# Optimization experiments

Measured on AMD Instinct MI355X. Metric: run time of the kernel, lower is better.

Reference implementation:

```python
import jax, jax.numpy as jnp
import numpy as np
from jax import lax

D = 64; B = 8; P = 16; E = P * (P - 1); C = 5; N = 256
H = 4; HD = D // H; NB = 5; NL = 2; NCLASSES = 8; NTYPES = 7


def _gelu(x):
    return jax.nn.gelu(x, approximate=False)


def _ln(x, g, b, eps=1e-5):
    m = x.mean(-1, keepdims=True)
    v = ((x - m) ** 2).mean(-1, keepdims=True)
    return (x - m) * lax.rsqrt(v + eps) * g + b


def _gn(x, g, b, groups=8, eps=1e-5):
    # x: [M, d, L]; GroupNorm over (channels_in_group, L)
    M, d, L = x.shape
    xg = x.reshape(M, groups, -1)
    m = xg.mean(-1, keepdims=True)
    v = ((xg - m) ** 2).mean(-1, keepdims=True)
    xg = (xg - m) * lax.rsqrt(v + eps)
    return xg.reshape(M, d, L) * g[None, :, None] + b[None, :, None]


def _forward(edge_data, edge_types, edge_mask, p, x_idx, y_idx, params):
    (stem_w, stem_b, conv_w, gn_g, gn_b, type_emb, em_w, em_b, em_g, em_bt,
     a_wqkv, a_bqkv, a_wo, a_bo, ln1_g, ln1_b, ff_w1, ff_b1, ff_w2, ff_b2,
     ln2_g, ln2_b, eh_w, eh_b, nm_w, nm_b, nm_g, nm_bt, nh_w, nh_b) = params
    Bq, Eq, Cq, Nq = edge_data.shape
    # --- EdgeFeatureExtractor: stem linear + 5 residual conv blocks + avg pool ---
    x = edge_data.reshape(Bq * Eq, Cq, Nq)
    h = jnp.einsum('mcn,cd->mdn', x, stem_w) + stem_b[None, :, None]  # [BE, d, N]
    for i in range(conv_w.shape[0]):
        c = lax.conv_general_dilated(h, conv_w[i], (1,), ((1, 1),),
                                     dimension_numbers=('NCH', 'OIH', 'NCH'))
        h = h + _gelu(_gn(c, gn_g[i], gn_b[i]))
    emb = h.mean(-1).reshape(Bq, Eq, D)  # adaptive avg pool to 1
    # --- type embedding + 2-input merge ---
    temb = type_emb[edge_types]
    emb = _gelu(_ln(jnp.concatenate([emb, temb], -1) @ em_w + em_b, em_g, em_bt))
    # --- 2 self-attention layers (post-LN) ---
    pad = ~edge_mask
    neg = jnp.asarray(-1e9, emb.dtype)
    scale = np.float32(1.0 / np.sqrt(HD))
    for l in range(a_wqkv.shape[0]):
        qkv = emb @ a_wqkv[l] + a_bqkv[l]
        q, k, v = jnp.split(qkv, 3, axis=-1)
        q = q.reshape(Bq, Eq, H, HD).transpose(0, 2, 1, 3)
        k = k.reshape(Bq, Eq, H, HD).transpose(0, 2, 1, 3)
        v = v.reshape(Bq, Eq, H, HD).transpose(0, 2, 1, 3)
        s = jnp.einsum('bhqd,bhkd->bhqk', q, k) * scale
        s = jnp.where(pad[:, None, None, :], neg, s)
        a = jax.nn.softmax(s, axis=-1)
        o = jnp.einsum('bhqk,bhkd->bhqd', a, v).transpose(0, 2, 1, 3).reshape(Bq, Eq, D)
        o = o @ a_wo[l] + a_bo[l]
        emb = _ln(emb + o, ln1_g[l], ln1_b[l])
        f = _gelu(emb @ ff_w1[l] + ff_b1[l]) @ ff_w2[l] + ff_b2[l]
        emb = _ln(emb + f, ln2_g[l], ln2_b[l])
    edge_logits = emb @ eh_w + eh_b  # [B, E, 2]
    # --- node heads: vectorized version of the per-node dict gather ---
    # edge_order[u, v] = u*(p-1) + v - (v > u)
    others = np.array([i for i in range(p) if i not in (x_idx, y_idx)], dtype=np.int64)

    def eidx(u, v):
        u = np.asarray(u); v = np.asarray(v)
        return u * (p - 1) + v - (v > u).astype(np.int64)

    i_ux = eidx(others, x_idx)
    i_uy = eidx(others, y_idx)
    i_xu = eidx(x_idx, others)
    i_yu = eidx(y_idx, others)
    g = jnp.concatenate([emb[:, i_ux], emb[:, i_uy], emb[:, i_xu], emb[:, i_yu]], axis=-1)  # [B, p-2, 4d]
    node = _gelu(_ln(g @ nm_w + nm_b, nm_g, nm_bt))
    node_logits = node @ nh_w + nh_b  # [B, p-2, 8]
    return edge_logits, node_logits


def setup_inputs() -> dict:
    key = jax.random.key(0)
    ks = iter(jax.random.split(key, 64))

    def rn(shape, s=0.05):
        return jax.random.normal(next(ks), shape, jnp.float32) * s

    return {
        'edge_data': jax.random.normal(next(ks), (B, E, C, N), jnp.float32),
        'edge_types': jax.random.randint(next(ks), (B, E), 0, NTYPES),
        'edge_mask': jnp.ones((B, E), dtype=bool),
        'p': P, 'x_idx': 0, 'y_idx': 1,
        'stem_w': rn((C, D)), 'stem_b': jnp.zeros((D,)),
        'conv_w': rn((NB, D, D, 3)), 'gn_g': jnp.ones((NB, D)), 'gn_b': jnp.zeros((NB, D)),
        'type_emb': rn((NTYPES, D), 1.0),
        'em_w': rn((2 * D, D)), 'em_b': jnp.zeros((D,)), 'em_g': jnp.ones((D,)), 'em_bt': jnp.zeros((D,)),
        'a_wqkv': rn((NL, D, 3 * D)), 'a_bqkv': jnp.zeros((NL, 3 * D)),
        'a_wo': rn((NL, D, D)), 'a_bo': jnp.zeros((NL, D)),
        'ln1_g': jnp.ones((NL, D)), 'ln1_b': jnp.zeros((NL, D)),
        'ff_w1': rn((NL, D, 4 * D)), 'ff_b1': jnp.zeros((NL, 4 * D)),
        'ff_w2': rn((NL, 4 * D, D)), 'ff_b2': jnp.zeros((NL, D)),
        'ln2_g': jnp.ones((NL, D)), 'ln2_b': jnp.zeros((NL, D)),
        'eh_w': rn((D, 2)), 'eh_b': jnp.zeros((2,)),
        'nm_w': rn((4 * D, D)), 'nm_b': jnp.zeros((D,)), 'nm_g': jnp.ones((D,)), 'nm_bt': jnp.zeros((D,)),
        'nh_w': rn((D, NCLASSES)), 'nh_b': jnp.zeros((NCLASSES,)),
    }


def reference(edge_data, edge_types, edge_mask, p, x_idx, y_idx, stem_w, stem_b,
              conv_w, gn_g, gn_b, type_emb, em_w, em_b, em_g, em_bt,
              a_wqkv, a_bqkv, a_wo, a_bo, ln1_g, ln1_b, ff_w1, ff_b1, ff_w2, ff_b2,
              ln2_g, ln2_b, eh_w, eh_b, nm_w, nm_b, nm_g, nm_bt, nh_w, nh_b):
    params = (stem_w, stem_b, conv_w, gn_g, gn_b, type_emb, em_w, em_b, em_g, em_bt,
              a_wqkv, a_bqkv, a_wo, a_bo, ln1_g, ln1_b, ff_w1, ff_b1, ff_w2, ff_b2,
              ln2_g, ln2_b, eh_w, eh_b, nm_w, nm_b, nm_g, nm_bt, nh_w, nh_b)
    return _forward(edge_data, edge_types, edge_mask, int(p), int(x_idx), int(y_idx), params)
```

## Files before the change

kernel.cpp:

```cpp
#include <hip/hip_runtime.h>
#include <hip/hip_bf16.h>
#include <math.h>

#define NEDGE 240
#define NBAT  8
#define MROWS 1920
#define NPTS  256
#define CIN   5

typedef __attribute__((ext_vector_type(8))) short  bf16x8;
typedef __attribute__((ext_vector_type(4))) float  f32x4;

__device__ __forceinline__ float gelu_f(float x){
    float x2 = x*x;
    float t  = fmaf(0.07135481f, x2, 1.59576912f);
    float s  = fminf(x*t, 80.f);
    float e  = __expf(s);
    float r  = __builtin_amdgcn_rcpf(e + 1.0f);
    return x*e*r;
}
__device__ __forceinline__ float wave_sum(float v){
    #pragma unroll
    for (int off=32; off>0; off>>=1) v += __shfl_xor(v, off);
    return v;
}
__device__ __forceinline__ unsigned short f2bf(float x){
    unsigned int u = __float_as_uint(x);
    return (unsigned short)((u + 0x7FFFu + ((u>>16)&1u)) >> 16);
}
__device__ __forceinline__ unsigned pack_bf2(float lo, float hi){
    __hip_bfloat162 t = __float22bfloat162_rn(make_float2(lo, hi));
    union { __hip_bfloat162 b; unsigned u; } cv; cv.b = t;
    return cv.u;
}

__global__ __launch_bounds__(256) void k_wprep(
    const float* __restrict__ conv_w, unsigned short* __restrict__ wf)
{
    int t = blockIdx.x*256 + threadIdx.x;
    if (t >= 120*64) return;
    int lane = t & 63, f = t >> 6;
    int q = f & 1, tap = (f>>1)%3, ob = (f/6)&3, layer = f/24;
    int o = 16*ob + (lane&15);
    int ibase = 32*q + 8*(lane>>4);
    #pragma unroll
    for (int e=0;e<8;++e){
        int i = ibase + e;
        float w = conv_w[(((size_t)layer*64 + o)*64 + i)*3 + tap];
        wf[(size_t)t*8 + e] = f2bf(w);
    }
}

__global__ __launch_bounds__(512, 2) void k_extract(
    const float* __restrict__ edge_data, const float* __restrict__ stem_w,
    const float* __restrict__ stem_b, const unsigned short* __restrict__ wf,
    const float* __restrict__ gn_g, const float* __restrict__ gn_b,
    float* __restrict__ emb0)
{
    __shared__ unsigned short hbf[258*64];
    __shared__ float redg[8][2][2];
    __shared__ float redp[8][16];
    __shared__ float gnp[640];
    const int m = blockIdx.x, tid = threadIdx.x;
    const int w = tid>>6, lane = tid&63;
    const int g = (lane>>4)&3, l15 = lane&15;
    const int wb = w&3, colbase = 128*(w>>2);
    const bf16x8* wfp = (const bf16x8*)wf;

    bf16x8 A[6];
    #pragma unroll
    for (int fq=0; fq<6; ++fq)
        A[fq] = wfp[(size_t)((wb*3)*2 + fq)*64 + lane];

    for (int i=tid; i<640; i+=512) gnp[i] = (i<320) ? gn_g[i] : gn_b[i-320];

    float h[8][4];

    {
        const float* xs = edge_data + (size_t)m*CIN*NPTS;
        float sw[4][6];
        #pragma unroll
        for (int j=0;j<4;++j){
            int o = 16*wb + 4*g + j;
            #pragma unroll
            for (int c=0;c<5;++c) sw[j][c] = stem_w[c*64+o];
            sw[j][5] = stem_b[o];
        }
        #pragma unroll
        for (int nbl=0;nbl<8;++nbl){
            int n = colbase + 16*nbl + l15;
            float x0=xs[n], x1=xs[NPTS+n], x2=xs[2*NPTS+n],
                  x3=xs[3*NPTS+n], x4=xs[4*NPTS+n];
            #pragma unroll
            for (int j=0;j<4;++j)
                h[nbl][j] = sw[j][5] + x0*sw[j][0] + x1*sw[j][1]
                          + x2*sw[j][2] + x3*sw[j][3] + x4*sw[j][4];
            int np = n + 1;
            #pragma unroll
            for (int jp=0;jp<2;++jp){
                int i0 = 16*wb + 4*g + 2*jp;
                unsigned off = (unsigned)(np*128 + (((i0>>3)^(np&7))<<4) + ((i0&7)<<1));
                *(unsigned*)((char*)hbf + off) = pack_bf2(h[nbl][2*jp], h[nbl][2*jp+1]);
            }
        }
    }
    if (tid < 32)       ((unsigned int*)hbf)[tid] = 0u;
    else if (tid < 64)  ((unsigned int*)hbf)[257*32 + tid - 32] = 0u;
    __syncthreads();

    #pragma unroll 1
    for (int layer=0; layer<5; ++layer){
        f32x4 acc[8];
        #pragma unroll
        for (int nbl=0;nbl<8;++nbl) acc[nbl] = (f32x4){0.f,0.f,0.f,0.f};

        #pragma unroll
        for (int tap=0; tap<3; ++tap)
        #pragma unroll
        for (int q=0; q<2; ++q){
            #pragma unroll
            for (int nbl=0;nbl<8;++nbl){
                int np = colbase + 16*nbl + l15 + tap;
                unsigned off = (unsigned)(np*128 + (((4*q+g)^(np&7))<<4));
                bf16x8 Bv = *(const bf16x8*)((const char*)hbf + off);
                acc[nbl] = __builtin_amdgcn_mfma_f32_16x16x32_bf16(
                               A[tap*2+q], Bv, acc[nbl], 0,0,0);
            }
        }

        float s=0.f, sq=0.f;
        #pragma unroll
        for (int nbl=0;nbl<8;++nbl)
            #pragma unroll
            for (int j=0;j<4;++j){ float v=acc[nbl][j]; s+=v; sq+=v*v; }
        #pragma unroll
        for (int off=1; off<=16; off<<=1){
            s  += __shfl_xor(s,  off);
            sq += __shfl_xor(sq, off);
        }
        if ((lane&31)==0){
            redg[w][lane>>5][0] = s;
            redg[w][lane>>5][1] = sq;
        }
        __syncthreads();

        if (layer < 4){
            #pragma unroll
            for (int fq=0; fq<6; ++fq)
                A[fq] = wfp[(size_t)((layer+1)*24 + (wb*3)*2 + fq)*64 + lane];
        }

        int hf = g>>1;
        float S = redg[wb][hf][0] + redg[wb+4][hf][0];
        float Q = redg[wb][hf][1] + redg[wb+4][hf][1];
        float mu = S*(1.f/2048.f);
        float rstd = rsqrtf(Q*(1.f/2048.f) - mu*mu + 1e-5f);

        float gg[4], bb[4];
        #pragma unroll
        for (int j=0;j<4;++j){
            int o = 16*wb + 4*g + j;
            gg[j] = gnp[layer*64+o]; bb[j] = gnp[320+layer*64+o];
        }
        #pragma unroll
        for (int nbl=0;nbl<8;++nbl)
            #pragma unroll
            for (int j=0;j<4;++j){
                float xn = (acc[nbl][j]-mu)*rstd*gg[j] + bb[j];
                h[nbl][j] += gelu_f(xn);
            }
        if (layer < 4){
            #pragma unroll
            for (int nbl=0;nbl<8;++nbl){
                int np = colbase + 16*nbl + l15 + 1;
                #pragma unroll
                for (int jp=0;jp<2;++jp){
                    int i0 = 16*wb + 4*g + 2*jp;
                    unsigned off = (unsigned)(np*128 + (((i0>>3)^(np&7))<<4) + ((i0&7)<<1));
                    *(unsigned*)((char*)hbf + off) = pack_bf2(h[nbl][2*jp], h[nbl][2*jp+1]);
                }
            }
            __syncthreads();
        }
    }

    float p[4];
    #pragma unroll
    for (int j=0;j<4;++j){
        float a = 0.f;
        #pragma unroll
        for (int nbl=0;nbl<8;++nbl) a += h[nbl][j];
        p[j] = a;
    }
    #pragma unroll
    for (int off=1; off<=8; off<<=1)
        #pragma unroll
        for (int j=0;j<4;++j) p[j] += __shfl_xor(p[j], off);
    if (l15==0){
        #pragma unroll
        for (int j=0;j<4;++j) redp[w][4*g+j] = p[j];
    }
    __syncthreads();
    if (tid < 64){
        int ob = tid>>4, r = tid&15;
        emb0[(size_t)m*64+tid] = (redp[ob][r] + redp[ob+4][r]) * (1.0f/256.0f);
    }
}

__global__ __launch_bounds__(256) void k_mergeqkv(
    const float* __restrict__ emb0, const int* __restrict__ edge_types,
    const float* __restrict__ type_emb, const float* __restrict__ em_w,
    const float* __restrict__ em_b, const float* __restrict__ em_g,
    const float* __restrict__ em_bt, const float* __restrict__ wqkv,
    const float* __restrict__ bqkv, float* __restrict__ emb,
    float* __restrict__ qkv)
{
    int m  = blockIdx.x*4 + (threadIdx.x>>6);
    int ln = threadIdx.x & 63;
    float a = emb0[(size_t)m*64+ln];
    int ty = edge_types[m];
    float tb = type_emb[ty*64+ln];
    float v = em_b[ln];
    for (int j=0;j<64;++j) v += __shfl(a,j)  * em_w[j*64+ln];
    for (int j=0;j<64;++j) v += __shfl(tb,j) * em_w[(64+j)*64+ln];
    float mu  = wave_sum(v)*(1.0f/64.0f);
    float d   = v - mu;
    float var = wave_sum(d*d)*(1.0f/64.0f);
    float e = gelu_f(d * rsqrtf(var+1e-5f) * em_g[ln] + em_bt[ln]);
    emb[(size_t)m*64+ln] = e;
    float q = bqkv[ln], k = bqkv[64+ln], vv = bqkv[128+ln];
    for (int j=0;j<64;++j){
        float ej = __shfl(e,j);
        q  += ej*wqkv[j*192+ln];
        k  += ej*wqkv[j*192+64+ln];
        vv += ej*wqkv[j*192+128+ln];
    }
    qkv[(size_t)m*192+ln]=q; qkv[(size_t)m*192+64+ln]=k; qkv[(size_t)m*192+128+ln]=vv;
}

__global__ __launch_bounds__(256) void k_attn(
    const float* __restrict__ qkv, float* __restrict__ o)
{
    __shared__ float Ks[NEDGE][16], Vs[NEDGE][16];
    int b = blockIdx.x >> 2, h = blockIdx.x & 3;
    int tid = threadIdx.x;
    for (int i=tid; i<NEDGE*16; i+=256){
        int r = i>>4, c = i&15;
        size_t base = ((size_t)(b*NEDGE+r))*192 + h*16 + c;
        Ks[r][c] = qkv[base+64];
        Vs[r][c] = qkv[base+128];
    }
    __syncthreads();
    if (tid < NEDGE){
        float qv[16];
        size_t qb = ((size_t)(b*NEDGE+tid))*192 + h*16;
        #pragma unroll
        for (int d=0; d<16; ++d) qv[d] = qkv[qb+d];
        float mx = -3e38f, l = 0.f, acc[16];
        #pragma unroll
        for (int d=0; d<16; ++d) acc[d]=0.f;
        for (int key=0; key<NEDGE; ++key){
            float s=0.f;
            #pragma unroll
            for (int d=0; d<16; ++d) s += qv[d]*Ks[key][d];
            s *= 0.25f;
            if (s > mx){
                float so = __expf(mx - s);
                l *= so;
                #pragma unroll
                for (int d=0; d<16; ++d) acc[d] *= so;
                mx = s;
            }
            float pp = __expf(s - mx);
            l += pp;
            #pragma unroll
            for (int d=0; d<16; ++d) acc[d] = fmaf(pp, Vs[key][d], acc[d]);
        }
        float inv = 1.f/l;
        size_t obase = ((size_t)(b*NEDGE+tid))*64 + h*16;
        #pragma unroll
        for (int d=0; d<16; ++d) o[obase+d] = acc[d]*inv;
    }
}

__global__ __launch_bounds__(256) void k_postattn(
    const float* __restrict__ o, const float* __restrict__ wo,
    const float* __restrict__ bo, const float* __restrict__ g1,
    const float* __restrict__ b1ln, const float* __restrict__ w1,
    const float* __restrict__ b1, const float* __restrict__ w2,
    const float* __restrict__ b2, const float* __restrict__ g2,
    const float* __restrict__ b2ln, float* __restrict__ emb,
    const float* __restrict__ wqkv, const float* __restrict__ bqkv,
    float* __restrict__ qkv)
{
    int m  = blockIdx.x*4 + (threadIdx.x>>6);
    int ln = threadIdx.x & 63;
    float ov = o[(size_t)m*64+ln];
    float r = bo[ln];
    for (int j=0;j<64;++j) r += __shfl(ov,j)*wo[j*64+ln];
    float x = emb[(size_t)m*64+ln] + r;
    float mu  = wave_sum(x)*(1.f/64.f);
    float d   = x-mu;
    float var = wave_sum(d*d)*(1.f/64.f);
    float e1 = d*rsqrtf(var+1e-5f)*g1[ln] + b1ln[ln];
    float h[4];
    #pragma unroll
    for (int u=0;u<4;++u) h[u]=b1[ln*4+u];
    for (int j=0;j<64;++j){
        float ej = __shfl(e1,j);
        const float* wr = w1 + j*256 + ln*4;
        #pragma unroll
        for (int u=0;u<4;++u) h[u] += ej*wr[u];
    }
    #pragma unroll
    for (int u=0;u<4;++u) h[u]=gelu_f(h[u]);
    float f = b2[ln];
    #pragma unroll
    for (int u=0;u<4;++u){
        for (int j=0;j<64;++j)
            f += __shfl(h[u],j) * w2[(j*4+u)*64+ln];
    }
    float x2 = e1 + f;
    float mu2  = wave_sum(x2)*(1.f/64.f);
    float d2   = x2-mu2;
    float var2 = wave_sum(d2*d2)*(1.f/64.f);
    float e2 = d2*rsqrtf(var2+1e-5f)*g2[ln] + b2ln[ln];
    emb[(size_t)m*64+ln] = e2;
    if (wqkv){
        float q = bqkv[ln], k = bqkv[64+ln], vv = bqkv[128+ln];
        for (int j=0;j<64;++j){
            float ej = __shfl(e2,j);
            q  += ej*wqkv[j*192+ln];
            k  += ej*wqkv[j*192+64+ln];
            vv += ej*wqkv[j*192+128+ln];
        }
        qkv[(size_t)m*192+ln]=q; qkv[(size_t)m*192+64+ln]=k; qkv[(size_t)m*192+128+ln]=vv;
    }
}

__global__ __launch_bounds__(256) void k_heads(
    const float* __restrict__ emb, const float* __restrict__ eh_w,
    const float* __restrict__ eh_b, const float* __restrict__ nm_w,
    const float* __restrict__ nm_b, const float* __restrict__ nm_g,
    const float* __restrict__ nm_bt, const float* __restrict__ nh_w,
    const float* __restrict__ nh_b, const int* __restrict__ pp,
    const int* __restrict__ xp, const int* __restrict__ yp,
    float* __restrict__ out)
{
    if (blockIdx.x < 15){
        int gid = blockIdx.x*256 + threadIdx.x;
        int m = gid>>1, c = gid&1;
        float s = eh_b[c];
        const float* e = emb + (size_t)m*64;
        #pragma unroll 8
        for (int j=0;j<64;++j) s += e[j]*eh_w[j*2+c];
        out[gid] = s;
        return;
    }
    int wid = (blockIdx.x-15)*4 + (threadIdx.x>>6);
    int ln  = threadIdx.x & 63;
    int p = pp[0], xi = xp[0], yi = yp[0];
    int nu = p-2;
    if (wid >= NBAT*nu) return;
    int b = wid / nu, r = wid % nu;
    int u=-1, cnt=0;
    for (int i=0;i<p;++i){ if (i!=xi && i!=yi){ if (cnt==r){u=i;break;} ++cnt; } }
    #define EIDX(a,v) ((a)*(p-1) + (v) - (((v)>(a))?1:0))
    int iux = EIDX(u,xi), iuy = EIDX(u,yi), ixu = EIDX(xi,u), iyu = EIDX(yi,u);
    float g0 = emb[((size_t)(b*NEDGE+iux))*64+ln];
    float g1 = emb[((size_t)(b*NEDGE+iuy))*64+ln];
    float g2 = emb[((size_t)(b*NEDGE+ixu))*64+ln];
    float g3 = emb[((size_t)(b*NEDGE+iyu))*64+ln];
    float v = nm_b[ln];
    for (int j=0;j<64;++j) v += __shfl(g0,j)*nm_w[j*64+ln];
    for (int j=0;j<64;++j) v += __shfl(g1,j)*nm_w[(64+j)*64+ln];
    for (int j=0;j<64;++j) v += __shfl(g2,j)*nm_w[(128+j)*64+ln];
    for (int j=0;j<64;++j) v += __shfl(g3,j)*nm_w[(192+j)*64+ln];
    float mu  = wave_sum(v)*(1.f/64.f);
    float d   = v-mu;
    float var = wave_sum(d*d)*(1.f/64.f);
    float node = gelu_f(d*rsqrtf(var+1e-5f)*nm_g[ln] + nm_bt[ln]);
    float pl[8];
    #pragma unroll
    for (int c=0;c<8;++c) pl[c] = node*nh_w[ln*8+c];
    #pragma unroll
    for (int off=32; off>0; off>>=1)
        #pragma unroll
        for (int c=0;c<8;++c) pl[c] += __shfl_xor(pl[c], off);
    if (ln==0){
        #pragma unroll
        for (int c=0;c<8;++c) out[MROWS*2 + ((size_t)wid)*8 + c] = pl[c] + nh_b[c];
    }
}

extern "C" void kernel_launch(void* const* d_in, const int* in_sizes, int n_in,
                              void* d_out, int out_size, void* d_ws, size_t ws_size,
                              hipStream_t stream)
{
    const float* edge_data = (const float*)d_in[0];
    const int*   edge_types= (const int*)d_in[1];
    const int* pp = (const int*)d_in[3];
    const int* xp = (const int*)d_in[4];
    const int* yp = (const int*)d_in[5];
    const float* stem_w=(const float*)d_in[6];
    const float* stem_b=(const float*)d_in[7];
    const float* conv_w=(const float*)d_in[8];
    const float* gn_g=(const float*)d_in[9];
    const float* gn_b=(const float*)d_in[10];
    const float* type_emb=(const float*)d_in[11];
    const float* em_w=(const float*)d_in[12];
    const float* em_b=(const float*)d_in[13];
    const float* em_g=(const float*)d_in[14];
    const float* em_bt=(const float*)d_in[15];
    const float* a_wqkv=(const float*)d_in[16];
    const float* a_bqkv=(const float*)d_in[17];
    const float* a_wo=(const float*)d_in[18];
    const float* a_bo=(const float*)d_in[19];
    const float* ln1_g=(const float*)d_in[20];
    const float* ln1_b=(const float*)d_in[21];
    const float* ff_w1=(const float*)d_in[22];
    const float* ff_b1=(const float*)d_in[23];
    const float* ff_w2=(const float*)d_in[24];
    const float* ff_b2=(const float*)d_in[25];
    const float* ln2_g=(const float*)d_in[26];
    const float* ln2_b=(const float*)d_in[27];
    const float* eh_w=(const float*)d_in[28];
    const float* eh_b=(const float*)d_in[29];
    const float* nm_w=(const float*)d_in[30];
    const float* nm_b=(const float*)d_in[31];
    const float* nm_g=(const float*)d_in[32];
    const float* nm_bt=(const float*)d_in[33];
    const float* nh_w=(const float*)d_in[34];
    const float* nh_b=(const float*)d_in[35];
    (void)in_sizes; (void)n_in; (void)out_size; (void)ws_size;

    unsigned short* wfrag = (unsigned short*)d_ws;
    float* wsf  = (float*)d_ws;
    float* emb  = wsf + 30720;
    float* qkvb = emb + 122880;
    float* obuf = qkvb + 368640;
    float* outp = (float*)d_out;

    k_wprep   <<<30, 256, 0, stream>>>(conv_w, wfrag);
    k_extract <<<MROWS, 512, 0, stream>>>(edge_data, stem_w, stem_b, wfrag, gn_g, gn_b, emb);
    k_mergeqkv<<<MROWS/4, 256, 0, stream>>>(emb, edge_types, type_emb, em_w, em_b, em_g,
                                            em_bt, a_wqkv, a_bqkv, emb, qkvb);
    k_attn    <<<NBAT*4, 256, 0, stream>>>(qkvb, obuf);
    k_postattn<<<MROWS/4, 256, 0, stream>>>(obuf, a_wo, a_bo, ln1_g, ln1_b,
                                            ff_w1, ff_b1, ff_w2, ff_b2, ln2_g, ln2_b,
                                            emb, a_wqkv + (size_t)64*192, a_bqkv + 192, qkvb);
    k_attn    <<<NBAT*4, 256, 0, stream>>>(qkvb, obuf);
    k_postattn<<<MROWS/4, 256, 0, stream>>>(obuf, a_wo + (size_t)64*64, a_bo + 64,
                                            ln1_g + 64, ln1_b + 64,
                                            ff_w1 + (size_t)64*256, ff_b1 + 256,
                                            ff_w2 + (size_t)256*64, ff_b2 + 64,
                                            ln2_g + 64, ln2_b + 64,
                                            emb, (const float*)nullptr, (const float*)nullptr, qkvb);
    k_heads   <<<43, 256, 0, stream>>>(emb, eh_w, eh_b, nm_w, nm_b, nm_g, nm_bt,
                                       nh_w, nh_b, pp, xp, yp, outp);
}
```

Before: 305.8 us.

## Split attention keys across lanes and streamline extract/post-attention kernels

The attention kernel now launches four times as many blocks. Each query is handled by four lanes that each scan a quarter of the keys, and their online-softmax states are merged with shuffles. K and V are stored transposed in shared memory. The conv extract kernel precomputes swizzled LDS addresses, writes 64-bit packed bf16 stores, moves the next layer's weight prefetch before the reduction barrier, and folds the GroupNorm affine into a single FMA. The merge and post-attention kernels split their dot-product accumulators and use float4 weight loads to shorten dependency chains; the transposed layout may add some LDS bank conflicts.

New measurement: 249.4 us. 18.4% less time.

```diff
diff --git a/kernel.cpp b/kernel.cpp
--- a/kernel.cpp
+++ b/kernel.cpp
@@ -70,9 +70,22 @@
     bf16x8 A[6];
     #pragma unroll
     for (int fq=0; fq<6; ++fq)
-        A[fq] = wfp[(size_t)((wb*3)*2 + fq)*64 + lane];
+        A[fq] = wfp[(size_t)(wb*6 + fq)*64 + lane];
 
     for (int i=tid; i<640; i+=512) gnp[i] = (i<320) ? gn_g[i] : gn_b[i-320];
+
+    const int i0 = 16*wb + 4*g;
+    unsigned raddr[3][2];
+    {
+        unsigned clb = (unsigned)((colbase + l15)*128);
+        #pragma unroll
+        for (int tap=0;tap<3;++tap)
+            #pragma unroll
+            for (int q=0;q<2;++q)
+                raddr[tap][q] = clb + (unsigned)(((4*q+g) ^ ((l15+tap)&7))<<4);
+    }
+    const unsigned wb0 = (unsigned)((colbase + l15 + 1)*128
+                       + (((i0>>3) ^ ((l15+1)&7))<<4) + ((i0&7)<<1));
 
     float h[8][4];
 
@@ -81,7 +94,7 @@
         float sw[4][6];
         #pragma unroll
         for (int j=0;j<4;++j){
-            int o = 16*wb + 4*g + j;
+            int o = i0 + j;
             #pragma unroll
             for (int c=0;c<5;++c) sw[j][c] = stem_w[c*64+o];
             sw[j][5] = stem_b[o];
@@ -95,13 +108,9 @@
             for (int j=0;j<4;++j)
                 h[nbl][j] = sw[j][5] + x0*sw[j][0] + x1*sw[j][1]
                           + x2*sw[j][2] + x3*sw[j][3] + x4*sw[j][4];
-            int np = n + 1;
-            #pragma unroll
-            for (int jp=0;jp<2;++jp){
-                int i0 = 16*wb + 4*g + 2*jp;
-                unsigned off = (unsigned)(np*128 + (((i0>>3)^(np&7))<<4) + ((i0&7)<<1));
-                *(unsigned*)((char*)hbf + off) = pack_bf2(h[nbl][2*jp], h[nbl][2*jp+1]);
-            }
+            unsigned long long pk = (unsigned long long)pack_bf2(h[nbl][0], h[nbl][1])
+                                  | ((unsigned long long)pack_bf2(h[nbl][2], h[nbl][3]) << 32);
+            *(unsigned long long*)((char*)hbf + wb0 + 2048*nbl) = pk;
         }
     }
     if (tid < 32)       ((unsigned int*)hbf)[tid] = 0u;
@@ -120,14 +129,19 @@
         for (int q=0; q<2; ++q){
             #pragma unroll
             for (int nbl=0;nbl<8;++nbl){
-                int np = colbase + 16*nbl + l15 + tap;
-                unsigned off = (unsigned)(np*128 + (((4*q+g)^(np&7))<<4));
-                bf16x8 Bv = *(const bf16x8*)((const char*)hbf + off);
+                bf16x8 Bv = *(const bf16x8*)((const char*)hbf
+                              + raddr[tap][q] + (2048*nbl + 128*tap));
                 acc[nbl] = __builtin_amdgcn_mfma_f32_16x16x32_bf16(
                                A[tap*2+q], Bv, acc[nbl], 0,0,0);
             }
         }
 
+        if (layer < 4){
+            #pragma unroll
+            for (int fq=0; fq<6; ++fq)
+                A[fq] = wfp[(size_t)((layer+1)*24 + wb*6 + fq)*64 + lane];
+        }
+
         float s=0.f, sq=0.f;
         #pragma unroll
         for (int nbl=0;nbl<8;++nbl)
@@ -143,12 +157,6 @@
             redg[w][lane>>5][1] = sq;
         }
         __syncthreads();
-
-        if (layer < 4){
-            #pragma unroll
-            for (int fq=0; fq<6; ++fq)
-                A[fq] = wfp[(size_t)((layer+1)*24 + (wb*3)*2 + fq)*64 + lane];
-        }
 
         int hf = g>>1;
         float S = redg[wb][hf][0] + redg[wb+4][hf][0];
@@ -156,29 +164,26 @@
         float mu = S*(1.f/2048.f);
         float rstd = rsqrtf(Q*(1.f/2048.f) - mu*mu + 1e-5f);
 
-        float gg[4], bb[4];
+        float K1[4], K2[4];
         #pragma unroll
         for (int j=0;j<4;++j){
-            int o = 16*wb + 4*g + j;
-            gg[j] = gnp[layer*64+o]; bb[j] = gnp[320+layer*64+o];
+            float gg = gnp[layer*64 + i0 + j], bb = gnp[320 + layer*64 + i0 + j];
+            K1[j] = rstd*gg;
+            K2[j] = fmaf(-mu, K1[j], bb);
         }
         #pragma unroll
         for (int nbl=0;nbl<8;++nbl)
             #pragma unroll
             for (int j=0;j<4;++j){
-                float xn = (acc[nbl][j]-mu)*rstd*gg[j] + bb[j];
+                float xn = fmaf(acc[nbl][j], K1[j], K2[j]);
                 h[nbl][j] += gelu_f(xn);
             }
         if (layer < 4){
             #pragma unroll
             for (int nbl=0;nbl<8;++nbl){
-                int np = colbase + 16*nbl + l15 + 1;
-                #pragma unroll
-                for (int jp=0;jp<2;++jp){
-                    int i0 = 16*wb + 4*g + 2*jp;
-                    unsigned off = (unsigned)(np*128 + (((i0>>3)^(np&7))<<4) + ((i0&7)<<1));
-                    *(unsigned*)((char*)hbf + off) = pack_bf2(h[nbl][2*jp], h[nbl][2*jp+1]);
-                }
+                unsigned long long pk = (unsigned long long)pack_bf2(h[nbl][0], h[nbl][1])
+                                      | ((unsigned long long)pack_bf2(h[nbl][2], h[nbl][3]) << 32);
+                *(unsigned long long*)((char*)hbf + wb0 + 2048*nbl) = pk;
             }
             __syncthreads();
         }
@@ -220,9 +225,10 @@
     float a = emb0[(size_t)m*64+ln];
     int ty = edge_types[m];
     float tb = type_emb[ty*64+ln];
-    float v = em_b[ln];
-    for (int j=0;j<64;++j) v += __shfl(a,j)  * em_w[j*64+ln];
-    for (int j=0;j<64;++j) v += __shfl(tb,j) * em_w[(64+j)*64+ln];
+    float va = 0.f, vb = 0.f;
+    for (int j=0;j<64;++j) va += __shfl(a,j)  * em_w[j*64+ln];
+    for (int j=0;j<64;++j) vb += __shfl(tb,j) * em_w[(64+j)*64+ln];
+    float v = em_b[ln] + va + vb;
     float mu  = wave_sum(v)*(1.0f/64.0f);
     float d   = v - mu;
     float var = wave_sum(d*d)*(1.0f/64.0f);
@@ -241,43 +247,63 @@
 __global__ __launch_bounds__(256) void k_attn(
     const float* __restrict__ qkv, float* __restrict__ o)
 {
-    __shared__ float Ks[NEDGE][16], Vs[NEDGE][16];
-    int b = blockIdx.x >> 2, h = blockIdx.x & 3;
+    __shared__ float KsT[16][244], VsT[16][244];
+    int blk = blockIdx.x;
+    int b  = blk >> 4;
+    int h  = (blk >> 2) & 3;
+    int qt = blk & 3;
     int tid = threadIdx.x;
     for (int i=tid; i<NEDGE*16; i+=256){
-        int r = i>>4, c = i&15;
-        size_t base = ((size_t)(b*NEDGE+r))*192 + h*16 + c;
-        Ks[r][c] = qkv[base+64];
-        Vs[r][c] = qkv[base+128];
+        int r = i>>4, d = i&15;
+        size_t base = ((size_t)(b*NEDGE+r))*192 + h*16 + d;
+        KsT[d][r] = qkv[base+64];
+        VsT[d][r] = qkv[base+128];
     }
     __syncthreads();
-    if (tid < NEDGE){
-        float qv[16];
-        size_t qb = ((size_t)(b*NEDGE+tid))*192 + h*16;
-        #pragma unroll
-        for (int d=0; d<16; ++d) qv[d] = qkv[qb+d];
-        float mx = -3e38f, l = 0.f, acc[16];
-        #pragma unroll
-        for (int d=0; d<16; ++d) acc[d]=0.f;
-        for (int key=0; key<NEDGE; ++key){
-            float s=0.f;
-            #pragma unroll
-            for (int d=0; d<16; ++d) s += qv[d]*Ks[key][d];
-            s *= 0.25f;
-            if (s > mx){
-                float so = __expf(mx - s);
-                l *= so;
-                #pragma unroll
-                for (int d=0; d<16; ++d) acc[d] *= so;
-                mx = s;
-            }
-            float pp = __expf(s - mx);
-            l += pp;
-            #pragma unroll
-            for (int d=0; d<16; ++d) acc[d] = fmaf(pp, Vs[key][d], acc[d]);
-        }
+    int c = tid & 3, qi = tid >> 2;
+    int q = qt*64 + qi;
+    bool act = (q < NEDGE);
+    float qv[16];
+    size_t qb = ((size_t)(b*NEDGE + (act ? q : 0)))*192 + h*16;
+    #pragma unroll
+    for (int d=0; d<16; ++d) qv[d] = qkv[qb+d];
+    float mx = -3e38f, l = 0.f, acc[16];
+    #pragma unroll
+    for (int d=0; d<16; ++d) acc[d]=0.f;
+    for (int k=0; k<60; ++k){
+        int key = 60*c + k;
+        float s=0.f;
+        #pragma unroll
+        for (int d=0; d<16; ++d) s += qv[d]*KsT[d][key];
+        s *= 0.25f;
+        if (s > mx){
+            float so = __expf(mx - s);
+            l *= so;
+            #pragma unroll
+            for (int d=0; d<16; ++d) acc[d] *= so;
+            mx = s;
+        }
+        float pp = __expf(s - mx);
+        l += pp;
+        #pragma unroll
+        for (int d=0; d<16; ++d) acc[d] = fmaf(pp, VsT[d][key], acc[d]);
+    }
+    #pragma unroll
+    for (int off=1; off<=2; off<<=1){
+        float mo = __shfl_xor(mx, off);
+        float lo = __shfl_xor(l,  off);
+        float M  = fmaxf(mx, mo);
+        float ss = __expf(mx - M);
+        float so = __expf(mo - M);
+        l = l*ss + lo*so;
+        #pragma unroll
+        for (int d=0; d<16; ++d)
+            acc[d] = acc[d]*ss + __shfl_xor(acc[d], off)*so;
+        mx = M;
+    }
+    if (act && c==0){
         float inv = 1.f/l;
-        size_t obase = ((size_t)(b*NEDGE+tid))*64 + h*16;
+        size_t obase = ((size_t)(b*NEDGE+q))*64 + h*16;
         #pragma unroll
         for (int d=0; d<16; ++d) o[obase+d] = acc[d]*inv;
     }
@@ -303,23 +329,23 @@
     float d   = x-mu;
     float var = wave_sum(d*d)*(1.f/64.f);
     float e1 = d*rsqrtf(var+1e-5f)*g1[ln] + b1ln[ln];
-    float h[4];
-    #pragma unroll
-    for (int u=0;u<4;++u) h[u]=b1[ln*4+u];
+    float4 bv = *(const float4*)(b1 + ln*4);
+    float h[4] = {bv.x, bv.y, bv.z, bv.w};
     for (int j=0;j<64;++j){
         float ej = __shfl(e1,j);
-        const float* wr = w1 + j*256 + ln*4;
-        #pragma unroll
-        for (int u=0;u<4;++u) h[u] += ej*wr[u];
+        float4 wv = *(const float4*)(w1 + j*256 + ln*4);
+        h[0] += ej*wv.x; h[1] += ej*wv.y; h[2] += ej*wv.z; h[3] += ej*wv.w;
     }
     #pragma unroll
     for (int u=0;u<4;++u) h[u]=gelu_f(h[u]);
-    float f = b2[ln];
-    #pragma unroll
-    for (int u=0;u<4;++u){
-        for (int j=0;j<64;++j)
-            f += __shfl(h[u],j) * w2[(j*4+u)*64+ln];
-    }
+    float f0=0.f, f1=0.f, f2=0.f, f3=0.f;
+    for (int j=0;j<64;++j){
+        f0 += __shfl(h[0],j) * w2[(j*4+0)*64+ln];
+        f1 += __shfl(h[1],j) * w2[(j*4+1)*64+ln];
+        f2 += __shfl(h[2],j) * w2[(j*4+2)*64+ln];
+        f3 += __shfl(h[3],j) * w2[(j*4+3)*64+ln];
+    }
+    float f = b2[ln] + ((f0+f1)+(f2+f3));
     float x2 = e1 + f;
     float mu2  = wave_sum(x2)*(1.f/64.f);
     float d2   = x2-mu2;
@@ -445,11 +471,11 @@
     k_extract <<<MROWS, 512, 0, stream>>>(edge_data, stem_w, stem_b, wfrag, gn_g, gn_b, emb);
     k_mergeqkv<<<MROWS/4, 256, 0, stream>>>(emb, edge_types, type_emb, em_w, em_b, em_g,
                                             em_bt, a_wqkv, a_bqkv, emb, qkvb);
-    k_attn    <<<NBAT*4, 256, 0, stream>>>(qkvb, obuf);
+    k_attn    <<<NBAT*16, 256, 0, stream>>>(qkvb, obuf);
     k_postattn<<<MROWS/4, 256, 0, stream>>>(obuf, a_wo, a_bo, ln1_g, ln1_b,
                                             ff_w1, ff_b1, ff_w2, ff_b2, ln2_g, ln2_b,
                                             emb, a_wqkv + (size_t)64*192, a_bqkv + 192, qkvb);
-    k_attn    <<<NBAT*4, 256, 0, stream>>>(qkvb, obuf);
+    k_attn    <<<NBAT*16, 256, 0, stream>>>(qkvb, obuf);
     k_postattn<<<MROWS/4, 256, 0, stream>>>(obuf, a_wo + (size_t)64*64, a_bo + 64,
                                             ln1_g + 64, ln1_b + 64,
                                             ff_w1 + (size_t)64*256, ff_b1 + 256,
```
